# Kernel optimization log

Hardware: AMD Instinct MI355X
Metric: run time of the kernel (lower is better)

## Reference

```python
import jax, jax.numpy as jnp
import numpy as np

B, T, D, H = 4, 1024, 1024, 16
HD = D // H
MAX_LEN = 1024


def _layernorm(x, g, b, eps=1e-5):
    mu = jnp.mean(x, axis=-1, keepdims=True)
    var = jnp.var(x, axis=-1, keepdims=True)
    return (x - mu) * jax.lax.rsqrt(var + eps) * g + b


def setup_inputs() -> dict:
    key = jax.random.key(0)
    ks = jax.random.split(key, 12)
    s = 1.0 / np.sqrt(D)
    return {
        "src": jax.random.normal(ks[0], (B, T, D), jnp.float32),
        "Wqkv": jax.random.uniform(ks[1], (D, 3 * D), jnp.float32, -s, s),
        "bqkv": jnp.zeros((3 * D,), jnp.float32),
        "Wo": jax.random.uniform(ks[2], (D, D), jnp.float32, -s, s),
        "bo": jnp.zeros((D,), jnp.float32),
        "rel_bias": 0.02 * jax.random.normal(ks[3], (H, 2 * MAX_LEN - 1), jnp.float32),
        "temperature": jnp.float32(1.0),
        "W1": jax.random.uniform(ks[4], (D, 4 * D), jnp.float32, -s, s),
        "b1": jnp.zeros((4 * D,), jnp.float32),
        "W2": jax.random.uniform(ks[5], (4 * D, D), jnp.float32, -1.0 / np.sqrt(4 * D), 1.0 / np.sqrt(4 * D)),
        "b2": jnp.zeros((D,), jnp.float32),
        "ff_scale": jnp.ones((1,), jnp.float32),
        "gamma1": jnp.ones((D,), jnp.float32),
        "beta1": jnp.zeros((D,), jnp.float32),
        "gamma2": jnp.ones((D,), jnp.float32),
        "beta2": jnp.zeros((D,), jnp.float32),
    }


def reference(src, Wqkv, bqkv, Wo, bo, rel_bias, temperature, W1, b1, W2, b2,
              ff_scale, gamma1, beta1, gamma2, beta2):
    b, t, c = src.shape
    # QKV projection -> [3, B, H, T, HD]
    qkv = (src @ Wqkv + bqkv).reshape(b, t, 3, H, HD).transpose(2, 0, 3, 1, 4)
    q, k, v = qkv[0], qkv[1], qkv[2]
    temp = jnp.maximum(temperature, 0.01)  # clamp(min=0.01)
    logits = jnp.einsum("bhqd,bhkd->bhqk", q, k) / temp
    # relative position bias gather: [H, T, T]
    pos = jnp.arange(t)
    rel = pos[None, :] - pos[:, None] + (t - 1)
    logits = logits + rel_bias[:, rel][None]
    attn_weights = jax.nn.softmax(logits, axis=-1)
    attn_out = jnp.einsum("bhqk,bhkd->bhqd", attn_weights, v)
    attn_out = attn_out.transpose(0, 2, 1, 3).reshape(b, t, c) @ Wo + bo
    x = _layernorm(src + attn_out, gamma1, beta1)
    ff = jax.nn.gelu(x @ W1 + b1, approximate=False) @ W2 + b2
    out = _layernorm(x + ff_scale * ff, gamma2, beta2)
    return (out, attn_weights)
```

## Files before the change

### kernel.cpp

```cpp
#include <hip/hip_runtime.h>
#include <math.h>

#define BB 4
#define TT 1024
#define DM 1024
#define NH 16
#define HD 64
#define DFF 4096
#define N3 3072

typedef unsigned short u16;
typedef __attribute__((ext_vector_type(4))) float f32x4;
typedef __attribute__((ext_vector_type(8))) short s16x8;

__device__ __forceinline__ u16 f2bf(float f) {
    union { float f; unsigned u; } v; v.f = f;
    unsigned u = v.u;
    u += 0x7fffu + ((u >> 16) & 1u);
    return (u16)(u >> 16);
}
__device__ __forceinline__ float bf2f(u16 h) {
    union { unsigned u; float f; } v; v.u = ((unsigned)h) << 16;
    return v.f;
}

__device__ __forceinline__ void async_copy16(const void* g, void* l) {
    __builtin_amdgcn_global_load_lds(
        (const __attribute__((address_space(1))) unsigned int*)g,
        (__attribute__((address_space(3))) unsigned int*)l, 16, 0, 0);
}

__global__ __launch_bounds__(256) void prep_kernel(const float* __restrict__ src,
                                                   u16* __restrict__ srcbf,
                                                   const float* __restrict__ Wqkv,
                                                   u16* __restrict__ WqkvT,
                                                   const float* __restrict__ Wo,
                                                   u16* __restrict__ WoT,
                                                   const float* __restrict__ W1,
                                                   u16* __restrict__ W1T,
                                                   const float* __restrict__ W2,
                                                   u16* __restrict__ W2T) {
    __shared__ float tile[32][33];
    int bid = blockIdx.x;
    int tid = threadIdx.x;
    if (bid < 4096) {
        int i = (bid * 256 + tid) * 4;
        float4 v = *(const float4*)(src + i);
        u16 pk[4] = {f2bf(v.x), f2bf(v.y), f2bf(v.z), f2bf(v.w)};
        *(uint2*)(srcbf + i) = *(uint2*)pk;
        return;
    }
    bid -= 4096;
    const float* in;
    u16* out;
    int R, C, bx, by;
    if (bid < 3072)        { in = Wqkv; out = WqkvT; R = DM;  C = N3;  bx = bid % 96;  by = bid / 96; }
    else if (bid < 4096)   { bid -= 3072; in = Wo; out = WoT; R = DM;  C = DM;  bx = bid % 32;  by = bid / 32; }
    else if (bid < 8192)   { bid -= 4096; in = W1; out = W1T; R = DM;  C = DFF; bx = bid % 128; by = bid / 128; }
    else                   { bid -= 8192; in = W2; out = W2T; R = DFF; C = DM;  bx = bid % 32;  by = bid / 32; }
    int c0 = bx * 32, r0 = by * 32;
    int tx = tid & 31, ty = tid >> 5;
    for (int i = 0; i < 4; i++)
        tile[ty + i * 8][tx] = in[(size_t)(r0 + ty + i * 8) * C + c0 + tx];
    __syncthreads();
    for (int i = 0; i < 4; i++)
        out[(size_t)(c0 + ty + i * 8) * R + r0 + tx] = f2bf(tile[tx][ty + i * 8]);
}

__global__ __launch_bounds__(256) void transpose_bf_kernel(const u16* __restrict__ inH,
                                                           u16* __restrict__ out, int R, int C) {
    __shared__ float tile[32][33];
    size_t boff = (size_t)blockIdx.z * R * C;
    int c0 = blockIdx.x * 32, r0 = blockIdx.y * 32;
    int tx = threadIdx.x & 31, ty = threadIdx.x >> 5;
    for (int i = 0; i < 4; i++) {
        int r = r0 + ty + i * 8, c = c0 + tx;
        tile[ty + i * 8][tx] = bf2f(inH[boff + (size_t)r * C + c]);
    }
    __syncthreads();
    for (int i = 0; i < 4; i++) {
        int rr = r0 + tx, cc = c0 + ty + i * 8;
        out[boff + (size_t)cc * R + rr] = f2bf(tile[tx][ty + i * 8]);
    }
}

template<int EPI, int NT>
__global__ __launch_bounds__(512, 2) void gemm256_kernel(const u16* __restrict__ A,
                                                         const u16* __restrict__ BT,
                                                         const float* __restrict__ bias,
                                                         void* __restrict__ out0v,
                                                         u16* __restrict__ out1,
                                                         u16* __restrict__ out2,
                                                         int M, int N, int Kstride) {
    __shared__ u16 As[4][8192];
    __shared__ u16 Bs[4][8192];
    const int tid = threadIdx.x;
    const int lane = tid & 63;
    const int wave = tid >> 6;
    const int quad = lane >> 4;
    const int l15 = lane & 15;
    const int wm = wave >> 2;
    const int wn = wave & 3;
    const int m0 = blockIdx.y * 256;
    const int n0 = blockIdx.x * 256;
    const int koff = blockIdx.z * (NT * 32);

    const int srow = wave * 32 + (lane >> 2);
    const int schunk = ((lane & 3) ^ ((lane >> 2) & 3)) * 8;
    const u16* aG0 = A + (size_t)(m0 + srow) * Kstride + koff + schunk;
    const u16* aG1 = aG0 + (size_t)16 * Kstride;
    const u16* bG0 = BT + (size_t)(n0 + srow) * Kstride + koff + schunk;
    const u16* bG1 = bG0 + (size_t)16 * Kstride;
    const int ldst0 = wave * 1024;
    const int ldst1 = wave * 1024 + 512;

#define STAGE_A(t) { int kk_ = (t) * 32; \
    async_copy16(aG0 + kk_, &As[(t) & 3][ldst0]); \
    async_copy16(aG1 + kk_, &As[(t) & 3][ldst1]); }
#define STAGE_B(t) { int kk_ = (t) * 32; \
    async_copy16(bG0 + kk_, &Bs[(t) & 3][ldst0]); \
    async_copy16(bG1 + kk_, &Bs[(t) & 3][ldst1]); }

    const int swq = (quad ^ (l15 & 3)) * 8;
    const int abase = (wm * 128 + l15) * 32 + swq;
    const int bbase = (wn * 64 + l15) * 32 + swq;

    f32x4 acc[8][4] = {};

    STAGE_A(0); STAGE_B(0);
    STAGE_A(1); STAGE_B(1);
    STAGE_A(2); STAGE_B(2);

#pragma unroll 1
    for (int t = 0; t < NT; ++t) {
        if (t < NT - 2)       asm volatile("s_waitcnt vmcnt(8)" ::: "memory");
        else if (t == NT - 2) asm volatile("s_waitcnt vmcnt(4)" ::: "memory");
        else                  asm volatile("s_waitcnt vmcnt(0)" ::: "memory");
        asm volatile("" ::: "memory");
        __builtin_amdgcn_s_barrier();
        asm volatile("" ::: "memory");

        const u16* as = As[t & 3];
        const u16* bs = Bs[t & 3];

        s16x8 bfr[4];
#pragma unroll
        for (int j = 0; j < 4; j++)
            bfr[j] = *(const s16x8*)&bs[bbase + j * 512];
        s16x8 afr[4];
#pragma unroll
        for (int i = 0; i < 4; i++)
            afr[i] = *(const s16x8*)&as[abase + i * 512];
        if (t + 3 < NT) STAGE_A(t + 3);
        __builtin_amdgcn_s_setprio(1);
#pragma unroll
        for (int i = 0; i < 4; i++)
#pragma unroll
            for (int j = 0; j < 4; j++)
                acc[i][j] = __builtin_amdgcn_mfma_f32_16x16x32_bf16(afr[i], bfr[j], acc[i][j], 0, 0, 0);
        __builtin_amdgcn_s_setprio(0);
#pragma unroll
        for (int i = 0; i < 4; i++)
            afr[i] = *(const s16x8*)&as[abase + 2048 + i * 512];
        if (t + 3 < NT) STAGE_B(t + 3);
        __builtin_amdgcn_s_setprio(1);
#pragma unroll
        for (int i = 0; i < 4; i++)
#pragma unroll
            for (int j = 0; j < 4; j++)
                acc[i + 4][j] = __builtin_amdgcn_mfma_f32_16x16x32_bf16(afr[i], bfr[j], acc[i + 4][j], 0, 0, 0);
        __builtin_amdgcn_s_setprio(0);
    }
#undef STAGE_A
#undef STAGE_B

    const size_t MN = (size_t)M * N;
#pragma unroll
    for (int i = 0; i < 8; i++) {
#pragma unroll
        for (int j = 0; j < 4; j++) {
            f32x4 c = acc[i][j];
            int gn = n0 + wn * 64 + j * 16 + l15;
            float bv = (EPI == 3) ? 0.f : bias[gn];
#pragma unroll
            for (int r = 0; r < 4; r++) {
                int gm = m0 + wm * 128 + i * 16 + quad * 4 + r;
                float v = c[r] + bv;
                if (EPI == 2) {
                    v = 0.5f * v * (1.f + erff(v * 0.70710678118f));
                    ((u16*)out0v)[(size_t)gm * N + gn] = f2bf(v);
                } else if (EPI == 3) {
                    ((float*)out0v)[(size_t)blockIdx.z * MN + (size_t)gm * N + gn] = v;
                } else {
                    int which = gn >> 10, h = (gn >> 6) & 15, d = gn & 63;
                    int bb = gm >> 10, tq = gm & 1023;
                    u16* dst = (which == 0) ? (u16*)out0v : ((which == 1) ? out1 : out2);
                    dst[((size_t)(bb * NH + h) * TT + tq) * HD + d] = f2bf(v);
                }
            }
        }
    }
}

__global__ __launch_bounds__(512) void attn_kernel(const u16* __restrict__ Qb,
                                                   const u16* __restrict__ Kb,
                                                   const u16* __restrict__ VTb,
                                                   const float* __restrict__ rel_bias,
                                                   const float* __restrict__ temp_p,
                                                   float* __restrict__ probs_out,
                                                   u16* __restrict__ attn_out) {
    __shared__ __align__(16) u16 Qs[16 * 72];
    __shared__ __align__(16) u16 Ps[16 * 1032];
    __shared__ float red[2][8][16];
    __shared__ float RB[1040];

    const int tid = threadIdx.x;
    const int lane = tid & 63, wave = tid >> 6, quad = lane >> 4, l15 = lane & 15;
    const int q0 = blockIdx.x * 16;
    const int h = blockIdx.y, b = blockIdx.z;
    const int bh = b * NH + h;
    const size_t headoff = (size_t)bh * TT * HD;

    float temp = fmaxf(temp_p[0], 0.01f);
    const float itemp = 1.f / temp;

    for (int i = tid; i < 1039; i += 512)
        RB[i] = rel_bias[h * 2047 + (1008 - q0) + i];
    if (tid < 256) {
        int row = tid >> 4, col = (tid & 15) * 4;
        const u16* srcp = Qb + headoff + (size_t)(q0 + row) * HD + col;
        *(uint2*)&Qs[row * 72 + col] = *(const uint2*)srcp;
    }
    __syncthreads();

    s16x8 a0 = *(const s16x8*)&Qs[l15 * 72 + quad * 8];
    s16x8 a1 = *(const s16x8*)&Qs[l15 * 72 + 32 + quad * 8];
    f32x4 s[8];
    const u16* Kh = Kb + headoff;
#pragma unroll
    for (int nt = 0; nt < 8; nt++) {
        int key = wave * 128 + nt * 16 + l15;
        const u16* kp = Kh + (size_t)key * HD;
        s16x8 b0 = *(const s16x8*)(kp + quad * 8);
        s16x8 b1 = *(const s16x8*)(kp + 32 + quad * 8);
        f32x4 acc = {};
        acc = __builtin_amdgcn_mfma_f32_16x16x32_bf16(a0, b0, acc, 0, 0, 0);
        acc = __builtin_amdgcn_mfma_f32_16x16x32_bf16(a1, b1, acc, 0, 0, 0);
#pragma unroll
        for (int r = 0; r < 4; r++)
            acc[r] = acc[r] * itemp + RB[key - (quad * 4 + r) + 15];
        s[nt] = acc;
    }

    float lm[4];
#pragma unroll
    for (int r = 0; r < 4; r++) {
        float m = s[0][r];
#pragma unroll
        for (int nt = 1; nt < 8; nt++) m = fmaxf(m, s[nt][r]);
        for (int off = 8; off >= 1; off >>= 1) m = fmaxf(m, __shfl_xor(m, off));
        lm[r] = m;
    }

    float ls[4] = {0.f, 0.f, 0.f, 0.f};
#pragma unroll
    for (int nt = 0; nt < 8; nt++)
#pragma unroll
        for (int r = 0; r < 4; r++) {
            float p = __expf(s[nt][r] - lm[r]);
            s[nt][r] = p;
            ls[r] += p;
        }
#pragma unroll
    for (int r = 0; r < 4; r++) {
        float v = ls[r];
        for (int off = 8; off >= 1; off >>= 1) v += __shfl_xor(v, off);
        ls[r] = v;
    }
    if (l15 == 0)
#pragma unroll
        for (int r = 0; r < 4; r++) {
            red[0][wave][quad * 4 + r] = lm[r];
            red[1][wave][quad * 4 + r] = ls[r];
        }
    __syncthreads();

    float fac[4];
#pragma unroll
    for (int r = 0; r < 4; r++) {
        int row = quad * 4 + r;
        float M = red[0][0][row];
#pragma unroll
        for (int w = 1; w < 8; w++) M = fmaxf(M, red[0][w][row]);
        float tot = 0.f;
#pragma unroll
        for (int w = 0; w < 8; w++) tot += __expf(red[0][w][row] - M) * red[1][w][row];
        fac[r] = __expf(lm[r] - M) / tot;
    }

    float* prow = probs_out + ((size_t)bh * TT + q0) * TT;
#pragma unroll
    for (int nt = 0; nt < 8; nt++) {
        int key = wave * 128 + nt * 16 + l15;
#pragma unroll
        for (int r = 0; r < 4; r++) {
            int row = quad * 4 + r;
            float pn = s[nt][r] * fac[r];
            prow[(size_t)row * TT + key] = pn;
            Ps[row * 1032 + key] = f2bf(pn);
        }
    }
    __syncthreads();

    f32x4 o[4] = {};
    const u16* Vh = VTb + headoff;
#pragma unroll
    for (int ks = 0; ks < 4; ks++) {
        int k0 = wave * 128 + ks * 32;
        s16x8 pa = *(const s16x8*)&Ps[l15 * 1032 + k0 + quad * 8];
#pragma unroll
        for (int nt = 0; nt < 4; nt++) {
            int d = nt * 16 + l15;
            s16x8 vb = *(const s16x8*)(Vh + (size_t)d * TT + k0 + quad * 8);
            o[nt] = __builtin_amdgcn_mfma_f32_16x16x32_bf16(pa, vb, o[nt], 0, 0, 0);
        }
    }
    __syncthreads();
    float* OpF = (float*)Ps;
#pragma unroll
    for (int nt = 0; nt < 4; nt++)
#pragma unroll
        for (int r = 0; r < 4; r++)
            OpF[(wave * 16 + quad * 4 + r) * 64 + nt * 16 + l15] = o[nt][r];
    __syncthreads();

    {
        int m = tid >> 5, dc = (tid & 31) * 2;
        float a0v = 0.f, a1v = 0.f;
#pragma unroll
        for (int w = 0; w < 8; w++) {
            a0v += OpF[(w * 16 + m) * 64 + dc];
            a1v += OpF[(w * 16 + m) * 64 + dc + 1];
        }
        u16 pk[2] = {f2bf(a0v), f2bf(a1v)};
        *(unsigned*)&attn_out[((size_t)(b * TT + q0 + m)) * DM + h * HD + dc] = *(unsigned*)pk;
    }
}

template<int MODE, int KS>
__global__ __launch_bounds__(256) void ln_kernel(const float* __restrict__ af32,
                                                 const u16* __restrict__ abf,
                                                 const float* __restrict__ part,
                                                 const float* __restrict__ biasN,
                                                 const float* __restrict__ scale_p,
                                                 const float* __restrict__ gamma,
                                                 const float* __restrict__ beta,
                                                 float* __restrict__ outf,
                                                 u16* __restrict__ outbf) {
    __shared__ float red[2][4];
    const size_t MN = (size_t)BB * TT * DM;
    int row = blockIdx.x;
    int tid = threadIdx.x;
    float sc = (MODE == 1) ? scale_p[0] : 1.f;
    int c0 = tid * 4;
    size_t base = (size_t)row * DM + c0;
    float4 a = *(const float4*)(biasN + c0);
    float acc[4] = {a.x, a.y, a.z, a.w};
#pragma unroll
    for (int kz = 0; kz < KS; kz++) {
        float4 p = *(const float4*)(part + kz * MN + base);
        acc[0] += p.x; acc[1] += p.y; acc[2] += p.z; acc[3] += p.w;
    }
    float x[4];
#pragma unroll
    for (int c = 0; c < 4; c++) {
        float b0 = (MODE == 0) ? af32[base + c] : bf2f(abf[base + c]);
        x[c] = b0 + sc * acc[c];
    }
    float s = x[0] + x[1] + x[2] + x[3];
    float sq = x[0] * x[0] + x[1] * x[1] + x[2] * x[2] + x[3] * x[3];
    for (int off = 32; off >= 1; off >>= 1) {
        s += __shfl_xor(s, off);
        sq += __shfl_xor(sq, off);
    }
    int wave = tid >> 6;
    if ((tid & 63) == 0) {
        red[0][wave] = s;
        red[1][wave] = sq;
    }
    __syncthreads();
    s = red[0][0] + red[0][1] + red[0][2] + red[0][3];
    sq = red[1][0] + red[1][1] + red[1][2] + red[1][3];
    float mu = s * (1.f / DM);
    float var = sq * (1.f / DM) - mu * mu;
    float rs = rsqrtf(var + 1e-5f);
#pragma unroll
    for (int c = 0; c < 4; c++) {
        float y = (x[c] - mu) * rs * gamma[c0 + c] + beta[c0 + c];
        if (MODE == 0) outbf[base + c] = f2bf(y);
        else outf[base + c] = y;
    }
}

#define OFF_SRCBF 0UL
#define OFF_WQKVT 8388608UL
#define OFF_WOT 14680064UL
#define OFF_W1T 16777216UL
#define OFF_W2T 25165824UL
#define OFF_Q 33554432UL
#define OFF_K 41943040UL
#define OFF_V 50331648UL
#define OFF_VT 58720256UL
#define OFF_ATTNO 67108864UL
#define OFF_XBF 83886080UL
#define OFF_H1 92274688UL
#define OFF_PART 134217728UL

extern "C" void kernel_launch(void* const* d_in, const int* in_sizes, int n_in,
                              void* d_out, int out_size, void* d_ws, size_t ws_size,
                              hipStream_t stream) {
    const float* src = (const float*)d_in[0];
    const float* Wqkv = (const float*)d_in[1];
    const float* bqkv = (const float*)d_in[2];
    const float* Wo = (const float*)d_in[3];
    const float* bo = (const float*)d_in[4];
    const float* relb = (const float*)d_in[5];
    const float* temp = (const float*)d_in[6];
    const float* W1 = (const float*)d_in[7];
    const float* b1 = (const float*)d_in[8];
    const float* W2 = (const float*)d_in[9];
    const float* b2 = (const float*)d_in[10];
    const float* ffs = (const float*)d_in[11];
    const float* g1 = (const float*)d_in[12];
    const float* be1 = (const float*)d_in[13];
    const float* g2 = (const float*)d_in[14];
    const float* be2 = (const float*)d_in[15];

    char* ws = (char*)d_ws;
    u16* srcbf = (u16*)(ws + OFF_SRCBF);
    u16* WqkvT = (u16*)(ws + OFF_WQKVT);
    u16* WoT = (u16*)(ws + OFF_WOT);
    u16* W1T = (u16*)(ws + OFF_W1T);
    u16* W2T = (u16*)(ws + OFF_W2T);
    u16* Qb = (u16*)(ws + OFF_Q);
    u16* Kb = (u16*)(ws + OFF_K);
    u16* Vb = (u16*)(ws + OFF_V);
    u16* VTb = (u16*)(ws + OFF_VT);
    u16* attnbf = (u16*)(ws + OFF_ATTNO);
    u16* xbf = (u16*)(ws + OFF_XBF);
    u16* h1bf = (u16*)(ws + OFF_H1);
    float* partF = (float*)(ws + OFF_PART);

    float* out_f = (float*)d_out;
    float* probs = out_f + (size_t)BB * TT * DM;

    prep_kernel<<<16384, 256, 0, stream>>>(src, srcbf, Wqkv, WqkvT, Wo, WoT,
                                           W1, W1T, W2, W2T);
    gemm256_kernel<1, 32><<<dim3(N3 / 256, (BB * TT) / 256, 1), 512, 0, stream>>>(
        srcbf, WqkvT, bqkv, Qb, Kb, Vb, BB * TT, N3, DM);
    transpose_bf_kernel<<<dim3(HD / 32, TT / 32, BB * NH), 256, 0, stream>>>(Vb, VTb, TT, HD);
    attn_kernel<<<dim3(TT / 16, NH, BB), 512, 0, stream>>>(Qb, Kb, VTb, relb, temp, probs, attnbf);
    gemm256_kernel<3, 8><<<dim3(DM / 256, (BB * TT) / 256, 4), 512, 0, stream>>>(
        attnbf, WoT, nullptr, partF, nullptr, nullptr, BB * TT, DM, DM);
    ln_kernel<0, 4><<<BB * TT, 256, 0, stream>>>(src, nullptr, partF, bo, nullptr, g1, be1,
                                                 nullptr, xbf);
    gemm256_kernel<2, 32><<<dim3(DFF / 256, (BB * TT) / 256, 1), 512, 0, stream>>>(
        xbf, W1T, b1, h1bf, nullptr, nullptr, BB * TT, DFF, DM);
    gemm256_kernel<3, 32><<<dim3(DM / 256, (BB * TT) / 256, 4), 512, 0, stream>>>(
        h1bf, W2T, nullptr, partF, nullptr, nullptr, BB * TT, DM, DFF);
    ln_kernel<1, 4><<<BB * TT, 256, 0, stream>>>(nullptr, xbf, partF, b2, ffs, g2, be2,
                                                 out_f, nullptr);
}
```

Measured before the change: 660.8 us.

## Restructure attention into per-wave two-pass softmax with streamed P·V

The attention kernel now gives each wave 16 query rows spanning all 1024 keys, instead of splitting keys across 8 waves and combining them through shared memory. A first pass over the keys computes the running max and sum online. A second pass recomputes the QK scores, normalizes them, writes the probabilities and feeds a small per-wave LDS tile straight into the P·V MFMA. This drops the large Ps buffer, the cross-wave reductions and several block barriers, and the MFMA operands are transposed so each lane writes contiguous probability chunks. The costs are computing QK twice, reading K from global memory twice, fewer and smaller blocks (lower occupancy), and probability outputs that are now bf16-rounded values widened to fp32.

```diff
diff --git a/kernel.cpp b/kernel.cpp
--- a/kernel.cpp
+++ b/kernel.cpp
@@ -202,148 +202,113 @@
     }
 }
 
-__global__ __launch_bounds__(512) void attn_kernel(const u16* __restrict__ Qb,
+__global__ __launch_bounds__(256) void attn_kernel(const u16* __restrict__ Qb,
                                                    const u16* __restrict__ Kb,
                                                    const u16* __restrict__ VTb,
                                                    const float* __restrict__ rel_bias,
                                                    const float* __restrict__ temp_p,
                                                    float* __restrict__ probs_out,
                                                    u16* __restrict__ attn_out) {
-    __shared__ __align__(16) u16 Qs[16 * 72];
-    __shared__ __align__(16) u16 Ps[16 * 1032];
-    __shared__ float red[2][8][16];
-    __shared__ float RB[1040];
+    __shared__ float RBs[1088];
+    __shared__ unsigned Pl[4][16 * 20];
 
     const int tid = threadIdx.x;
-    const int lane = tid & 63, wave = tid >> 6, quad = lane >> 4, l15 = lane & 15;
-    const int q0 = blockIdx.x * 16;
+    const int lane = tid & 63, wid = tid >> 6, quad = lane >> 4, l15 = lane & 15;
+    const int q0b = blockIdx.x * 64;
     const int h = blockIdx.y, b = blockIdx.z;
     const int bh = b * NH + h;
     const size_t headoff = (size_t)bh * TT * HD;
 
-    float temp = fmaxf(temp_p[0], 0.01f);
-    const float itemp = 1.f / temp;
-
-    for (int i = tid; i < 1039; i += 512)
-        RB[i] = rel_bias[h * 2047 + (1008 - q0) + i];
-    if (tid < 256) {
-        int row = tid >> 4, col = (tid & 15) * 4;
-        const u16* srcp = Qb + headoff + (size_t)(q0 + row) * HD + col;
-        *(uint2*)&Qs[row * 72 + col] = *(const uint2*)srcp;
-    }
+    const float itemp = 1.f / fmaxf(temp_p[0], 0.01f);
+
+    for (int i = tid; i < 1087; i += 256)
+        RBs[i] = rel_bias[h * 2047 + (960 - q0b) + i];
     __syncthreads();
 
-    s16x8 a0 = *(const s16x8*)&Qs[l15 * 72 + quad * 8];
-    s16x8 a1 = *(const s16x8*)&Qs[l15 * 72 + 32 + quad * 8];
-    f32x4 s[8];
+    const int qloc = wid * 16 + l15;
+    const int qg = q0b + qloc;
+    const u16* qp = Qb + headoff + (size_t)qg * HD;
+    const s16x8 qa0 = *(const s16x8*)(qp + quad * 8);
+    const s16x8 qa1 = *(const s16x8*)(qp + 32 + quad * 8);
+
     const u16* Kh = Kb + headoff;
-#pragma unroll
-    for (int nt = 0; nt < 8; nt++) {
-        int key = wave * 128 + nt * 16 + l15;
-        const u16* kp = Kh + (size_t)key * HD;
-        s16x8 b0 = *(const s16x8*)(kp + quad * 8);
-        s16x8 b1 = *(const s16x8*)(kp + 32 + quad * 8);
-        f32x4 acc = {};
-        acc = __builtin_amdgcn_mfma_f32_16x16x32_bf16(a0, b0, acc, 0, 0, 0);
-        acc = __builtin_amdgcn_mfma_f32_16x16x32_bf16(a1, b1, acc, 0, 0, 0);
-#pragma unroll
-        for (int r = 0; r < 4; r++)
-            acc[r] = acc[r] * itemp + RB[key - (quad * 4 + r) + 15];
-        s[nt] = acc;
-    }
-
-    float lm[4];
-#pragma unroll
-    for (int r = 0; r < 4; r++) {
-        float m = s[0][r];
-#pragma unroll
-        for (int nt = 1; nt < 8; nt++) m = fmaxf(m, s[nt][r]);
-        for (int off = 8; off >= 1; off >>= 1) m = fmaxf(m, __shfl_xor(m, off));
-        lm[r] = m;
-    }
-
-    float ls[4] = {0.f, 0.f, 0.f, 0.f};
-#pragma unroll
-    for (int nt = 0; nt < 8; nt++)
-#pragma unroll
-        for (int r = 0; r < 4; r++) {
-            float p = __expf(s[nt][r] - lm[r]);
-            s[nt][r] = p;
-            ls[r] += p;
+    const int rbo = 63 - qloc;
+
+    float m = -3.0e38f, l = 0.f;
+#pragma unroll 2
+    for (int kt = 0; kt < 64; kt++) {
+        const u16* kp = Kh + (size_t)(kt * 16 + l15) * HD;
+        s16x8 ka0 = *(const s16x8*)(kp + quad * 8);
+        s16x8 ka1 = *(const s16x8*)(kp + 32 + quad * 8);
+        f32x4 sv = {};
+        sv = __builtin_amdgcn_mfma_f32_16x16x32_bf16(ka0, qa0, sv, 0, 0, 0);
+        sv = __builtin_amdgcn_mfma_f32_16x16x32_bf16(ka1, qa1, sv, 0, 0, 0);
+        int kb = kt * 16 + quad * 4 + rbo;
+        float v0 = sv[0] * itemp + RBs[kb + 0];
+        float v1 = sv[1] * itemp + RBs[kb + 1];
+        float v2 = sv[2] * itemp + RBs[kb + 2];
+        float v3 = sv[3] * itemp + RBs[kb + 3];
+        float tm = fmaxf(fmaxf(v0, v1), fmaxf(v2, v3));
+        float mn = fmaxf(m, tm);
+        float c = __expf(m - mn);
+        l = l * c + __expf(v0 - mn) + __expf(v1 - mn) + __expf(v2 - mn) + __expf(v3 - mn);
+        m = mn;
+    }
+    float M = fmaxf(m, __shfl_xor(m, 16));
+    M = fmaxf(M, __shfl_xor(M, 32));
+    float la = l * __expf(m - M);
+    la += __shfl_xor(la, 16);
+    la += __shfl_xor(la, 32);
+    const float inv = 1.f / la;
+
+    f32x4 o[4] = {};
+    unsigned* Pw = Pl[wid];
+    const u16* Vh = VTb + headoff;
+    float* prow = probs_out + ((size_t)bh * TT + qg) * TT;
+
+#pragma unroll 1
+    for (int c2 = 0; c2 < 32; c2++) {
+        int k0 = c2 * 32;
+#pragma unroll
+        for (int t = 0; t < 2; t++) {
+            int kt = 2 * c2 + t;
+            const u16* kp = Kh + (size_t)(kt * 16 + l15) * HD;
+            s16x8 ka0 = *(const s16x8*)(kp + quad * 8);
+            s16x8 ka1 = *(const s16x8*)(kp + 32 + quad * 8);
+            f32x4 sv = {};
+            sv = __builtin_amdgcn_mfma_f32_16x16x32_bf16(ka0, qa0, sv, 0, 0, 0);
+            sv = __builtin_amdgcn_mfma_f32_16x16x32_bf16(ka1, qa1, sv, 0, 0, 0);
+            int kb = kt * 16 + quad * 4 + rbo;
+            float p0 = __expf(sv[0] * itemp + RBs[kb + 0] - M) * inv;
+            float p1 = __expf(sv[1] * itemp + RBs[kb + 1] - M) * inv;
+            float p2 = __expf(sv[2] * itemp + RBs[kb + 2] - M) * inv;
+            float p3 = __expf(sv[3] * itemp + RBs[kb + 3] - M) * inv;
+            unsigned w0 = (unsigned)f2bf(p0) | ((unsigned)f2bf(p1) << 16);
+            unsigned w1 = (unsigned)f2bf(p2) | ((unsigned)f2bf(p3) << 16);
+            Pw[l15 * 20 + t * 8 + quad * 2 + 0] = w0;
+            Pw[l15 * 20 + t * 8 + quad * 2 + 1] = w1;
         }
-#pragma unroll
-    for (int r = 0; r < 4; r++) {
-        float v = ls[r];
-        for (int off = 8; off >= 1; off >>= 1) v += __shfl_xor(v, off);
-        ls[r] = v;
-    }
-    if (l15 == 0)
-#pragma unroll
-        for (int r = 0; r < 4; r++) {
-            red[0][wave][quad * 4 + r] = lm[r];
-            red[1][wave][quad * 4 + r] = ls[r];
+        s16x8 pb = *(const s16x8*)&Pw[l15 * 20 + quad * 4];
+        f32x4 f0, f1;
+#pragma unroll
+        for (int j = 0; j < 4; j++) {
+            f0[j] = bf2f((u16)pb[j]);
+            f1[j] = bf2f((u16)pb[4 + j]);
         }
-    __syncthreads();
-
-    float fac[4];
-#pragma unroll
-    for (int r = 0; r < 4; r++) {
-        int row = quad * 4 + r;
-        float M = red[0][0][row];
-#pragma unroll
-        for (int w = 1; w < 8; w++) M = fmaxf(M, red[0][w][row]);
-        float tot = 0.f;
-#pragma unroll
-        for (int w = 0; w < 8; w++) tot += __expf(red[0][w][row] - M) * red[1][w][row];
-        fac[r] = __expf(lm[r] - M) / tot;
-    }
-
-    float* prow = probs_out + ((size_t)bh * TT + q0) * TT;
-#pragma unroll
-    for (int nt = 0; nt < 8; nt++) {
-        int key = wave * 128 + nt * 16 + l15;
-#pragma unroll
-        for (int r = 0; r < 4; r++) {
-            int row = quad * 4 + r;
-            float pn = s[nt][r] * fac[r];
-            prow[(size_t)row * TT + key] = pn;
-            Ps[row * 1032 + key] = f2bf(pn);
+        *(f32x4*)(prow + k0 + quad * 8) = f0;
+        *(f32x4*)(prow + k0 + quad * 8 + 4) = f1;
+#pragma unroll
+        for (int nt = 0; nt < 4; nt++) {
+            s16x8 va = *(const s16x8*)(Vh + (size_t)(nt * 16 + l15) * TT + k0 + quad * 8);
+            o[nt] = __builtin_amdgcn_mfma_f32_16x16x32_bf16(va, pb, o[nt], 0, 0, 0);
         }
     }
-    __syncthreads();
-
-    f32x4 o[4] = {};
-    const u16* Vh = VTb + headoff;
-#pragma unroll
-    for (int ks = 0; ks < 4; ks++) {
-        int k0 = wave * 128 + ks * 32;
-        s16x8 pa = *(const s16x8*)&Ps[l15 * 1032 + k0 + quad * 8];
-#pragma unroll
-        for (int nt = 0; nt < 4; nt++) {
-            int d = nt * 16 + l15;
-            s16x8 vb = *(const s16x8*)(Vh + (size_t)d * TT + k0 + quad * 8);
-            o[nt] = __builtin_amdgcn_mfma_f32_16x16x32_bf16(pa, vb, o[nt], 0, 0, 0);
-        }
-    }
-    __syncthreads();
-    float* OpF = (float*)Ps;
-#pragma unroll
-    for (int nt = 0; nt < 4; nt++)
-#pragma unroll
-        for (int r = 0; r < 4; r++)
-            OpF[(wave * 16 + quad * 4 + r) * 64 + nt * 16 + l15] = o[nt][r];
-    __syncthreads();
-
-    {
-        int m = tid >> 5, dc = (tid & 31) * 2;
-        float a0v = 0.f, a1v = 0.f;
-#pragma unroll
-        for (int w = 0; w < 8; w++) {
-            a0v += OpF[(w * 16 + m) * 64 + dc];
-            a1v += OpF[(w * 16 + m) * 64 + dc + 1];
-        }
-        u16 pk[2] = {f2bf(a0v), f2bf(a1v)};
-        *(unsigned*)&attn_out[((size_t)(b * TT + q0 + m)) * DM + h * HD + dc] = *(unsigned*)pk;
+
+    u16* aout = attn_out + ((size_t)(b * TT + qg)) * DM + h * HD;
+#pragma unroll
+    for (int nt = 0; nt < 4; nt++) {
+        u16 pk[4] = {f2bf(o[nt][0]), f2bf(o[nt][1]), f2bf(o[nt][2]), f2bf(o[nt][3])};
+        *(uint2*)(aout + nt * 16 + quad * 4) = *(uint2*)pk;
     }
 }
 
@@ -459,7 +424,7 @@
     gemm256_kernel<1, 32><<<dim3(N3 / 256, (BB * TT) / 256, 1), 512, 0, stream>>>(
         srcbf, WqkvT, bqkv, Qb, Kb, Vb, BB * TT, N3, DM);
     transpose_bf_kernel<<<dim3(HD / 32, TT / 32, BB * NH), 256, 0, stream>>>(Vb, VTb, TT, HD);
-    attn_kernel<<<dim3(TT / 16, NH, BB), 512, 0, stream>>>(Qb, Kb, VTb, relb, temp, probs, attnbf);
+    attn_kernel<<<dim3(TT / 64, NH, BB), 256, 0, stream>>>(Qb, Kb, VTb, relb, temp, probs, attnbf);
     gemm256_kernel<3, 8><<<dim3(DM / 256, (BB * TT) / 256, 4), 512, 0, stream>>>(
         attnbf, WoT, nullptr, partF, nullptr, nullptr, BB * TT, DM, DM);
     ln_kernel<0, 4><<<BB * TT, 256, 0, stream>>>(src, nullptr, partF, bo, nullptr, g1, be1,
```

Result: slower. 698.9 us (+5.8%).
